# Optimization experiments

Measured on AMD Instinct MI355X. Metric: run time of the kernel, lower is better.

The kernel has to match this reference:

```python
import jax, jax.numpy as jnp
import numpy as np

EPS = 1e-6
NEG = -100000.0


def _ln(x):
    # LayerNorm, elementwise_affine=False, eps=1e-6
    mu = jnp.mean(x, axis=-1, keepdims=True)
    var = jnp.mean((x - mu) ** 2, axis=-1, keepdims=True)
    return (x - mu) * jax.lax.rsqrt(var + EPS)


def _split_heads(x, h):
    b, s, d = x.shape
    return x.reshape(b, s, h, d // h).transpose(0, 2, 1, 3)  # [B,H,S,Dh]


def _merge_heads(x):
    b, h, s, dh = x.shape
    return x.transpose(0, 2, 1, 3).reshape(b, s, h * dh)


def _conv_pool(x, w):
    # grouped Conv2d(num_heads -> num_heads, kernel=(4,1), stride=(4,1), groups=num_heads, bias=False)
    # x: [B,H,S,Dh] as NCHW, w: [H,1,4,1] as OIHW
    return jax.lax.conv_general_dilated(
        x, w, window_strides=(4, 1), padding='VALID',
        dimension_numbers=('NCHW', 'OIHW', 'NCHW'),
        feature_group_count=x.shape[1])


def setup_inputs() -> dict:
    key = jax.random.key(0)
    ks = jax.random.split(key, 14)
    B, S, M, D, QKV, MLP, H = 4, 4096, 256, 768, 768, 3072, 12
    std = 0.02
    f = lambda k, shp: jax.random.normal(k, shp, jnp.float32) * std
    return {
        'x': jax.random.normal(ks[0], (B, S, D), jnp.float32),
        'memory': jax.random.normal(ks[1], (B, M, D), jnp.float32),
        'mask': jax.random.randint(ks[2], (B, S), 0, 2).astype(jnp.int32),
        'Wq': f(ks[3], (QKV, D)), 'Wk': f(ks[4], (QKV, D)),
        'Wv': f(ks[5], (QKV, D)), 'Wo': f(ks[6], (D, QKV)),
        'conv_w': f(ks[7], (H, 1, 4, 1)),
        'Uq': f(ks[8], (QKV, D)), 'Uk': f(ks[9], (QKV, D)),
        'Uv': f(ks[10], (QKV, D)), 'Uo': f(ks[11], (D, QKV)),
        'W1': f(ks[12], (MLP, D)), 'W2': f(ks[13], (D, MLP)),
    }


def reference(x, memory, mask, Wq, Wk, Wv, Wo, conv_w, Uq, Uk, Uv, Uo, W1, W2):
    H = conv_w.shape[0]
    maskf = mask.astype(x.dtype)                       # [B,S]

    # ---- pack: ConvAttention(memory as q, x as k/v); conv downsamples k/v ->
    #      shape_change=True so the k_mask is skipped (as in the torch code).
    q = _split_heads(memory @ Wq.T, H)                 # [B,H,M,Dh], unit temperature (log_temp=0)
    k = _split_heads(x @ Wk.T, H)                      # [B,H,S,Dh]
    v = _split_heads(x @ Wv.T, H)
    k = _conv_pool(k, conv_w)                          # [B,H,S//4,Dh]
    v = _conv_pool(v, conv_w)
    logits = jnp.einsum('bhqd,bhkd->bhqk', q, k)
    att = jax.nn.softmax(logits, axis=-1)
    packed = _merge_heads(att @ v) @ Wo.T              # [B,M,D]

    # ---- unpack: TAttention(x as q, packed as k/v) with q_mask injection
    head_dim = Uq.shape[0] // H
    uq = _split_heads(x @ Uq.T, H) * (1.0 / jnp.sqrt(jnp.asarray(head_dim, x.dtype)))
    uk = _split_heads(packed @ Uk.T, H)                # [B,H,M,Dh]
    uv = _split_heads(packed @ Uv.T, H)
    ulogits = jnp.einsum('bhqd,bhkd->bhqk', uq, uk)    # [B,H,S,M]
    ulogits = ulogits + NEG * (1.0 - maskf[:, None, :, None])
    uatt = jax.nn.softmax(ulogits, axis=-1)
    unpacked = _merge_heads(uatt @ uv) @ Uo.T          # [B,S,D]

    unpacked = unpacked * maskf[..., None]
    q_out = _ln(x + unpacked)
    m_out = _ln(memory + packed)

    # FFN: Linear -> GELU(exact) -> Linear (dropout=0)
    h = jax.nn.gelu(jnp.einsum('bsd,md->bsm', q_out, W1), approximate=False)
    y = jnp.einsum('bsm,dm->bsd', h, W2)
    y = y * maskf[..., None]
    q_out = _ln(q_out + y)
    return (q_out, m_out)
```

## Files before the change

### kernel.cpp

```cpp
#include <hip/hip_runtime.h>
#include <hip/hip_bf16.h>
#include <math.h>


typedef unsigned short u16;
typedef __attribute__((ext_vector_type(8))) short bf8v;
typedef __attribute__((ext_vector_type(4))) float f4v;
typedef __attribute__((ext_vector_type(4))) unsigned short us4v;

#define AS1 __attribute__((address_space(1)))
#define AS3 __attribute__((address_space(3)))

__device__ __forceinline__ void gld_lds16(const void* g, void* l) {
  __builtin_amdgcn_global_load_lds((const AS1 unsigned int*)g,
                                   (AS3 unsigned int*)l, 16, 0, 0);
}

__device__ __forceinline__ u16 bf16_rne(float x) {
  unsigned u = __float_as_uint(x);
  return (u16)((u + 0x7fffu + ((u >> 16) & 1u)) >> 16);
}
__device__ __forceinline__ float bf16_to_f(u16 h) {
  return __uint_as_float(((unsigned)h) << 16);
}

__global__ __launch_bounds__(256) void tobf16_kernel(
    const float* __restrict__ in, u16* __restrict__ o, int n4) {
  int i = blockIdx.x * 256 + threadIdx.x;
  if (i >= n4) return;
  float4 v = ((const float4*)in)[i];
  us4v h;
  h[0] = bf16_rne(v.x); h[1] = bf16_rne(v.y);
  h[2] = bf16_rne(v.z); h[3] = bf16_rne(v.w);
  ((us4v*)o)[i] = h;
}

template <int BN, int GELU, int OMODE>
__global__ __launch_bounds__(256) void bgemm_kernel(
    const u16* __restrict__ A, const u16* __restrict__ B,
    float* __restrict__ Cf, u16* __restrict__ Cb, int M, int N, int K,
    int lda, int ldb, int ldc, long long aSB, long long aSH, long long bSB,
    long long bSH, long long cSB, long long cSH, int HB, float scale) {
  constexpr int NJ = BN / 32;
  constexpr int LPB = BN / 64;
  __shared__ u16 smA[2][4096];
  __shared__ u16 smB[2][BN * 32];
  const int t = threadIdx.x;
  const int w = t >> 6, lane = t & 63;
  const int z = blockIdx.z;
  const int bb = z / HB, hh = z % HB;
  const u16* Ab = A + bb * aSB + hh * aSH;
  const u16* Bb = B + bb * bSB + hh * bSH;
  float* Cfb = (OMODE != 1) ? (Cf + bb * cSB + hh * cSH) : nullptr;
  u16* Cbb = (OMODE >= 1) ? (Cb + bb * cSB + hh * cSH) : nullptr;

  const int gx = gridDim.x;
  const int nwg = gx * gridDim.y;
  int f = blockIdx.x + gx * blockIdx.y;
  if ((nwg & 7) == 0) {
    const int cpx = nwg >> 3;
    f = (f & 7) * cpx + (f >> 3);
  }
  const int row0 = (f / gx) * 128, col0 = (f % gx) * BN;

  const int brow_l = lane >> 2;
  const int bchunk = ((lane & 3) ^ ((lane >> 3) & 3)) * 8;
  const int fr = lane & 15;
  const int fq = lane >> 4;
  const int fco = (fq ^ ((lane >> 1) & 3)) * 8;
  const int wr = (w >> 1) * 64, wc = (w & 1) * (BN / 2);

  f4v acc[4][NJ];
#pragma unroll
  for (int i = 0; i < 4; ++i)
#pragma unroll
    for (int j = 0; j < NJ; ++j) acc[i][j] = {0.f, 0.f, 0.f, 0.f};

  const int NT = K >> 5;

#pragma unroll
  for (int i = 0; i < 2; ++i) {
    const int g = w * 2 + i;
    const int r = g * 16 + brow_l;
    gld_lds16(Ab + (long long)(row0 + r) * lda + bchunk,
              &smA[0][g * 512 + lane * 8]);
  }
#pragma unroll
  for (int i = 0; i < LPB; ++i) {
    const int g = w * LPB + i;
    const int r = g * 16 + brow_l;
    gld_lds16(Bb + (long long)(col0 + r) * ldb + bchunk,
              &smB[0][g * 512 + lane * 8]);
  }
  __syncthreads();

  for (int tt = 0; tt < NT; ++tt) {
    const int cur = tt & 1, nxt = cur ^ 1;
    const bool more = (tt + 1) < NT;
    if (more) {
      const int k1 = (tt + 1) << 5;
#pragma unroll
      for (int i = 0; i < 2; ++i) {
        const int g = w * 2 + i;
        const int r = g * 16 + brow_l;
        gld_lds16(Ab + (long long)(row0 + r) * lda + k1 + bchunk,
                  &smA[nxt][g * 512 + lane * 8]);
      }
#pragma unroll
      for (int i = 0; i < LPB; ++i) {
        const int g = w * LPB + i;
        const int r = g * 16 + brow_l;
        gld_lds16(Bb + (long long)(col0 + r) * ldb + k1 + bchunk,
                  &smB[nxt][g * 512 + lane * 8]);
      }
    }
    {
      bf8v af[4], bfr[NJ];
#pragma unroll
      for (int mi = 0; mi < 4; ++mi)
        af[mi] = *(const bf8v*)&smA[cur][(wr + mi * 16 + fr) * 32 + fco];
#pragma unroll
      for (int nj = 0; nj < NJ; ++nj)
        bfr[nj] = *(const bf8v*)&smB[cur][(wc + nj * 16 + fr) * 32 + fco];
#pragma unroll
      for (int mi = 0; mi < 4; ++mi)
#pragma unroll
        for (int nj = 0; nj < NJ; ++nj)
          acc[mi][nj] = __builtin_amdgcn_mfma_f32_16x16x32_bf16(
              af[mi], bfr[nj], acc[mi][nj], 0, 0, 0);
    }
    __syncthreads();
  }

#pragma unroll
  for (int mi = 0; mi < 4; ++mi)
#pragma unroll
    for (int nj = 0; nj < NJ; ++nj) {
      const int col = col0 + wc + nj * 16 + fr;
      const long long base =
          (long long)(row0 + wr + mi * 16 + fq * 4) * ldc + col;
#pragma unroll
      for (int j = 0; j < 4; ++j) {
        float v = acc[mi][nj][j] * scale;
        if (GELU) v = 0.5f * v * (1.f + erff(v * 0.70710678118654752f));
        const long long idx = base + (long long)j * ldc;
        if (OMODE != 1) Cfb[idx] = v;
        if (OMODE >= 1) Cbb[idx] = bf16_rne(v);
      }
    }
}

__global__ __launch_bounds__(512) void fused_unpack_attn(
    const u16* __restrict__ q, const u16* __restrict__ k,
    const u16* __restrict__ vt, u16* __restrict__ o) {
  __shared__ char pool[76800];
  u16* smA = (u16*)pool;
  u16* smB = (u16*)(pool + 8192);
  u16* Pbuf = (u16*)pool;
  u16* smV = (u16*)(pool + 65536);
  float* partial = (float*)(pool + 73728);
  float* rowmax = (float*)(pool + 75776);
  float* rowsum = (float*)(pool + 76288);

  const int t = threadIdx.x;
  const int w = t >> 6, lane = t & 63;
  const int z = blockIdx.z;
  const int b = z / 12, h = z % 12;
  const int q0 = blockIdx.x * 128;

  const long long qoff = ((long long)b * 4096 + q0) * 768 + h * 64;
  const long long koff = ((long long)b * 256) * 768 + h * 64;
  const long long vbase = ((long long)(b * 12 + h)) * 16384;

  const int fr = lane & 15, fq = lane >> 4;
  const int fco = (fq ^ ((lane >> 1) & 3)) * 8;
  const int brow_l = lane >> 2;
  const int bchunk = ((lane & 3) ^ ((lane >> 3) & 3)) * 8;

  const int wr = (w >> 2) * 64, wc = (w & 3) * 64;
  f4v acc[4][4];
#pragma unroll
  for (int i = 0; i < 4; ++i)
#pragma unroll
    for (int j = 0; j < 4; ++j) acc[i][j] = {0.f, 0.f, 0.f, 0.f};

  for (int k0 = 0; k0 < 64; k0 += 32) {
    __syncthreads();
#pragma unroll
    for (int i = 0; i < 2; ++i) {
      const int g = w * 2 + i;
      const int r = g * 16 + brow_l;
      gld_lds16(k + koff + (long long)r * 768 + k0 + bchunk,
                smB + g * 512 + lane * 8);
    }
    {
      const int r = w * 16 + brow_l;
      gld_lds16(q + qoff + (long long)r * 768 + k0 + bchunk,
                smA + w * 512 + lane * 8);
    }
    __syncthreads();
#pragma unroll
    for (int mi = 0; mi < 4; ++mi) {
      const bf8v a0 = *(const bf8v*)&smA[(wr + mi * 16 + fr) * 32 + fco];
#pragma unroll
      for (int nj = 0; nj < 4; ++nj) {
        const bf8v b0 = *(const bf8v*)&smB[(wc + nj * 16 + fr) * 32 + fco];
        acc[mi][nj] = __builtin_amdgcn_mfma_f32_16x16x32_bf16(a0, b0, acc[mi][nj], 0, 0, 0);
      }
    }
  }
  __syncthreads();

  if (w < 4) {
    const int r = w * 16 + brow_l;
    gld_lds16(vt + vbase + (long long)r * 256 + bchunk,
              smV + w * 512 + lane * 8);
  }

#pragma unroll
  for (int mi = 0; mi < 4; ++mi)
#pragma unroll
    for (int j = 0; j < 4; ++j) {
      float m = fmaxf(fmaxf(acc[mi][0][j], acc[mi][1][j]),
                      fmaxf(acc[mi][2][j], acc[mi][3][j]));
#pragma unroll
      for (int o2 = 1; o2 < 16; o2 <<= 1) m = fmaxf(m, __shfl_xor(m, o2));
      if (fr == 0) partial[(w & 3) * 128 + wr + mi * 16 + fq * 4 + j] = m;
    }
  __syncthreads();
  if (t < 128)
    rowmax[t] = fmaxf(fmaxf(partial[t], partial[128 + t]),
                      fmaxf(partial[256 + t], partial[384 + t]));
  __syncthreads();
#pragma unroll
  for (int mi = 0; mi < 4; ++mi)
#pragma unroll
    for (int j = 0; j < 4; ++j) {
      const int row = wr + mi * 16 + fq * 4 + j;
      const float rm = rowmax[row];
      float s = 0.f;
#pragma unroll
      for (int nj = 0; nj < 4; ++nj) {
        const float e = exp2f(acc[mi][nj][j] - rm);
        s += e;
        const int col = wc + nj * 16 + fr;
        const int kc = col >> 5, kloc = col & 31;
        Pbuf[kc * 4096 + row * 32 + (((kloc >> 3) ^ ((row >> 1) & 3)) * 8) +
             (kloc & 7)] = bf16_rne(e);
      }
#pragma unroll
      for (int o2 = 1; o2 < 16; o2 <<= 1) s += __shfl_xor(s, o2);
      if (fr == 0) partial[(w & 3) * 128 + row] = s;
    }
  __syncthreads();
  if (t < 128)
    rowsum[t] = 1.f / ((partial[t] + partial[128 + t]) +
                       (partial[256 + t] + partial[384 + t]));
  __syncthreads();

  const int wrp = (w >> 1) * 32, wcp = (w & 1) * 32;
  f4v acc2[2][2];
#pragma unroll
  for (int i = 0; i < 2; ++i)
#pragma unroll
    for (int j = 0; j < 2; ++j) acc2[i][j] = {0.f, 0.f, 0.f, 0.f};

  for (int kc = 0; kc < 8; ++kc) {
    const int cur = (kc & 1) * 2048;
    if (kc < 7 && w < 4) {
      const int r = w * 16 + brow_l;
      gld_lds16(vt + vbase + (long long)r * 256 + (kc + 1) * 32 + bchunk,
                smV + (2048 - cur) + w * 512 + lane * 8);
    }
#pragma unroll
    for (int mi = 0; mi < 2; ++mi) {
      const bf8v pa =
          *(const bf8v*)&Pbuf[kc * 4096 + (wrp + mi * 16 + fr) * 32 + fco];
#pragma unroll
      for (int nj = 0; nj < 2; ++nj) {
        const bf8v v0 =
            *(const bf8v*)&smV[cur + (wcp + nj * 16 + fr) * 32 + fco];
        acc2[mi][nj] = __builtin_amdgcn_mfma_f32_16x16x32_bf16(pa, v0, acc2[mi][nj], 0, 0, 0);
      }
    }
    __syncthreads();
  }
#pragma unroll
  for (int mi = 0; mi < 2; ++mi)
#pragma unroll
    for (int nj = 0; nj < 2; ++nj)
#pragma unroll
      for (int j = 0; j < 4; ++j) {
        const int row = wrp + mi * 16 + fq * 4 + j;
        const int col = wcp + nj * 16 + fr;
        o[qoff + (long long)row * 768 + col] =
            bf16_rne(acc2[mi][nj][j] * rowsum[row]);
      }
}

__global__ __launch_bounds__(256) void conv_bf16_kernel(
    const u16* __restrict__ in, const float* __restrict__ w,
    u16* __restrict__ o, int total, int ld) {
  int idx = blockIdx.x * 256 + threadIdx.x;
  if (idx >= total) return;
  const int dh = idx & 63;
  int r = idx >> 6;
  const int tt = r & 1023; r >>= 10;
  const int h = r % 12;
  const int b = r / 12;
  const long long s = ((long long)(b * 4096 + 4 * tt)) * ld + h * 64 + dh;
  const float* wh = w + h * 4;
  float v = 0.f;
#pragma unroll
  for (int j = 0; j < 4; ++j) v = fmaf(wh[j], bf16_to_f(in[s + j * ld]), v);
  o[idx] = bf16_rne(v);
}

__global__ __launch_bounds__(256) void convT_bf16_kernel(
    const u16* __restrict__ in, const float* __restrict__ w,
    u16* __restrict__ o, int total, int ld) {
  int idx = blockIdx.x * 256 + threadIdx.x;
  if (idx >= total) return;
  const int tt = idx & 1023;
  int r = idx >> 10;
  const int dh = r & 63; r >>= 6;
  const int h = r % 12;
  const int b = r / 12;
  const long long s = ((long long)(b * 4096 + 4 * tt)) * ld + h * 64 + dh;
  const float* wh = w + h * 4;
  float v = 0.f;
#pragma unroll
  for (int j = 0; j < 4; ++j) v = fmaf(wh[j], bf16_to_f(in[s + j * ld]), v);
  o[idx] = bf16_rne(v);
}

__global__ __launch_bounds__(256) void transT_bf16_kernel(
    const float* __restrict__ in, u16* __restrict__ o, int total) {
  int idx = blockIdx.x * 256 + threadIdx.x;
  if (idx >= total) return;
  const int key = idx & 255;
  int r = idx >> 8;
  const int dh = r & 63; r >>= 6;
  const int h = r % 12;
  const int b = r / 12;
  o[idx] = bf16_rne(in[((long long)(b * 256 + key)) * 768 + h * 64 + dh]);
}

__global__ __launch_bounds__(256) void softmax_bf16_kernel(
    const float* __restrict__ in, u16* __restrict__ ob) {
  const long long row = blockIdx.x;
  const float* p = in + row * 1024;
  const int t = threadIdx.x;
  __shared__ float red[4];
  float v[4];
  float lmax = -3.4e38f;
#pragma unroll
  for (int i = 0; i < 4; ++i) {
    v[i] = p[t + (i << 8)];
    lmax = fmaxf(lmax, v[i]);
  }
  for (int o = 32; o; o >>= 1) lmax = fmaxf(lmax, __shfl_xor(lmax, o));
  if ((t & 63) == 0) red[t >> 6] = lmax;
  __syncthreads();
  const float gmax = fmaxf(fmaxf(red[0], red[1]), fmaxf(red[2], red[3]));
  float lsum = 0.f;
#pragma unroll
  for (int i = 0; i < 4; ++i) {
    v[i] = expf(v[i] - gmax);
    lsum += v[i];
  }
  __syncthreads();
  for (int o = 32; o; o >>= 1) lsum += __shfl_xor(lsum, o);
  if ((t & 63) == 0) red[t >> 6] = lsum;
  __syncthreads();
  const float inv = 1.f / (red[0] + red[1] + red[2] + red[3]);
#pragma unroll
  for (int i = 0; i < 4; ++i)
    ob[row * 1024 + t + (i << 8)] = bf16_rne(v[i] * inv);
}

__global__ __launch_bounds__(256) void ln_kernel(
    const float* __restrict__ a, const float* __restrict__ b,
    const int* __restrict__ mask, float* __restrict__ out,
    u16* __restrict__ outb) {
  const long long row = blockIdx.x;
  const float* pa = a + row * 768;
  const float* pb = b + row * 768;
  const float ms = mask ? (float)mask[row] : 1.f;
  __shared__ float buf[768];
  __shared__ float red[4];
  const int t = threadIdx.x;
  float lsum = 0.f;
#pragma unroll
  for (int i = t; i < 768; i += 256) {
    const float v = fmaf(pb[i], ms, pa[i]);
    buf[i] = v;
    lsum += v;
  }
  for (int o = 32; o; o >>= 1) lsum += __shfl_xor(lsum, o);
  if ((t & 63) == 0) red[t >> 6] = lsum;
  __syncthreads();
  const float mu = (red[0] + red[1] + red[2] + red[3]) * (1.f / 768.f);
  float lvar = 0.f;
#pragma unroll
  for (int i = t; i < 768; i += 256) {
    const float d = buf[i] - mu;
    lvar = fmaf(d, d, lvar);
  }
  __syncthreads();
  for (int o = 32; o; o >>= 1) lvar += __shfl_xor(lvar, o);
  if ((t & 63) == 0) red[t >> 6] = lvar;
  __syncthreads();
  const float var = (red[0] + red[1] + red[2] + red[3]) * (1.f / 768.f);
  const float rstd = rsqrtf(var + 1e-6f);
  float* po = out + row * 768;
  u16* pob = outb ? outb + row * 768 : nullptr;
#pragma unroll
  for (int i = t; i < 768; i += 256) {
    const float v = (buf[i] - mu) * rstd;
    po[i] = v;
    if (outb) pob[i] = bf16_rne(v);
  }
}

static inline void tobf16(hipStream_t st, const float* in, u16* o, int n) {
  int n4 = n / 4;
  tobf16_kernel<<<(n4 + 255) / 256, 256, 0, st>>>(in, o, n4);
}

extern "C" void kernel_launch(void* const* d_in, const int* in_sizes, int n_in,
                              void* d_out, int out_size, void* d_ws,
                              size_t ws_size, hipStream_t stream) {
  const float* x = (const float*)d_in[0];
  const float* memory = (const float*)d_in[1];
  const int* mask = (const int*)d_in[2];
  const float* Wq = (const float*)d_in[3];
  const float* Wk = (const float*)d_in[4];
  const float* Wv = (const float*)d_in[5];
  const float* Wo = (const float*)d_in[6];
  const float* conv_w = (const float*)d_in[7];
  const float* Uq = (const float*)d_in[8];
  const float* Uk = (const float*)d_in[9];
  const float* Uv = (const float*)d_in[10];
  const float* Uo = (const float*)d_in[11];
  const float* W1 = (const float*)d_in[12];
  const float* W2 = (const float*)d_in[13];
  float* out = (float*)d_out;
  float* ws = (float*)d_ws;

  const int XR = 16384, MR = 1024, D = 768, MLP = 3072;
  const long long CB = 3145728;
  const int WD = 589824;
  const int WM = 2359296;

  float* slotA = ws + 0;
  float* slotB = ws + 12582912;
  float* slotC = ws + 25165824;
  float* X     = ws + 28311552;
  float* s0    = ws + 34603008;
  float* s1    = ws + 35389440;
  float* s2    = ws + 36175872;
  float* s3    = ws + 36962304;
  float* s4    = ws + 37748736;
  float* Wp    = ws + 38535168;

  u16* kvb  = (u16*)slotA;
  u16* xb   = (u16*)slotB;
  u16* attb = (u16*)(slotB + 6291456);
  u16* uqb  = (u16*)(slotB + 6291456);
  u16* uattvb = (u16*)slotA;
  u16* qout1b = (u16*)(out + 6291456);
  u16* hb   = (u16*)slotA;
  float* ybuf = slotC;
  u16* qpb  = (u16*)s0;
  u16* memb = qpb + 786432;
  u16* avmb = (u16*)s1;
  u16* pkb  = avmb + 786432;
  float* packed = s2;
  u16* ukbb = (u16*)s3;
  u16* uvTb = ukbb + 786432;
  float* uvb = s4;
  u16* kpb  = (u16*)X;
  u16* vpTb = kpb + 3145728;
  u16* wp16 = (u16*)Wp;
  u16* Wkvb = wp16;
  u16* Wqb = wp16 + 2 * WD;
  u16* Wob = wp16 + 3 * WD;
  u16 *Uqb = wp16, *Ukb = wp16 + WD, *Uvb = wp16 + 2 * WD, *Uob = wp16 + 3 * WD;
  u16 *W1b = wp16, *W2b = wp16 + WM;

  tobf16(stream, x, xb, 12582912);
  tobf16(stream, memory, memb, 786432);
  tobf16(stream, Wk, Wkvb, WD);
  tobf16(stream, Wv, Wkvb + WD, WD);
  tobf16(stream, Wq, Wqb, WD);
  tobf16(stream, Wo, Wob, WD);
  bgemm_kernel<128, 0, 1><<<dim3(12, 128, 1), 256, 0, stream>>>(
      xb, Wkvb, nullptr, kvb, XR, 1536, D, D, D, 1536,
      0, 0, 0, 0, 0, 0, 1, 1.f);
  bgemm_kernel<128, 0, 1><<<dim3(6, 8, 1), 256, 0, stream>>>(
      memb, Wqb, nullptr, qpb, MR, D, D, D, D, D, 0, 0, 0, 0, 0, 0, 1, 1.f);
  conv_bf16_kernel<<<12288, 256, 0, stream>>>(kvb, conv_w, kpb, 3145728, 1536);
  convT_bf16_kernel<<<12288, 256, 0, stream>>>(kvb + 768, conv_w, vpTb, 3145728, 1536);
  bgemm_kernel<128, 0, 0><<<dim3(8, 2, 48), 256, 0, stream>>>(
      qpb, kpb, slotA, nullptr, 256, 1024, 64, 768, 64, 1024,
      196608, 64, 786432, 65536, 3145728, 262144, 12, 1.f);
  softmax_bf16_kernel<<<12288, 256, 0, stream>>>(slotA, attb);
  bgemm_kernel<64, 0, 1><<<dim3(1, 2, 48), 256, 0, stream>>>(
      attb, vpTb, nullptr, avmb, 256, 64, 1024, 1024, 1024, 768,
      3145728, 262144, 786432, 65536, 196608, 64, 12, 1.f);
  bgemm_kernel<128, 0, 2><<<dim3(6, 8, 1), 256, 0, stream>>>(
      avmb, Wob, packed, pkb, MR, D, D, D, D, D, 0, 0, 0, 0, 0, 0, 1, 1.f);
  ln_kernel<<<MR, 256, 0, stream>>>(memory, packed, nullptr, out + 12582912,
                                    nullptr);

  tobf16(stream, Uq, Uqb, WD);
  tobf16(stream, Uk, Ukb, WD);
  tobf16(stream, Uv, Uvb, WD);
  tobf16(stream, Uo, Uob, WD);
  bgemm_kernel<128, 0, 1><<<dim3(6, 128, 1), 256, 0, stream>>>(
      xb, Uqb, nullptr, uqb, XR, D, D, D, D, D, 0, 0, 0, 0, 0, 0, 1,
      0.18033688011112042592f);
  bgemm_kernel<128, 0, 1><<<dim3(6, 8, 1), 256, 0, stream>>>(
      pkb, Ukb, nullptr, ukbb, MR, D, D, D, D, D, 0, 0, 0, 0, 0, 0, 1, 1.f);
  bgemm_kernel<128, 0, 0><<<dim3(6, 8, 1), 256, 0, stream>>>(
      pkb, Uvb, uvb, nullptr, MR, D, D, D, D, D, 0, 0, 0, 0, 0, 0, 1, 1.f);
  transT_bf16_kernel<<<3072, 256, 0, stream>>>(uvb, uvTb, 786432);
  {
    dim3 g(32, 1, 48);
    fused_unpack_attn<<<g, 512, 0, stream>>>(uqb, ukbb, uvTb, uattvb);
  }
  bgemm_kernel<128, 0, 0><<<dim3(6, 32, 4), 256, 0, stream>>>(
      uattvb, Uob, slotB, nullptr, 4096, D, D, D, D, D,
      CB, 0, 0, 0, CB, 0, 1, 1.f);
  ln_kernel<<<XR, 256, 0, stream>>>(x, slotB, mask, slotB, qout1b);

  tobf16(stream, W1, W1b, WM);
  tobf16(stream, W2, W2b, WM);
  for (int c = 0; c < 2; ++c) {
    bgemm_kernel<128, 1, 1><<<dim3(24, 32, 2), 256, 0, stream>>>(
        qout1b + (long long)c * 2 * 3145728, W1b, nullptr, hb, 4096, MLP, D,
        D, D, MLP, 3145728, 0, 0, 0, 12582912, 0, 1, 1.f);
    bgemm_kernel<64, 0, 0><<<dim3(12, 32, 2), 256, 0, stream>>>(
        hb, W2b, ybuf, nullptr, 4096, D, MLP, MLP, MLP, D,
        12582912, 0, 0, 0, 3145728, 0, 1, 1.f);
    ln_kernel<<<8192, 256, 0, stream>>>(slotB + (long long)c * 2 * CB, ybuf,
                                        mask + c * 8192,
                                        out + (long long)c * 2 * CB, nullptr);
  }
}
```

Baseline: 720.9 us.

## Fuse Uq projection into KV GEMM, merge Uk/Uv GEMMs, in-place softmax, retile FFN

Concatenates Wk, Wv and a pre-scaled Uq into a single 2304-wide weight so one GEMM over x produces k, v and the unpack query together, and merges the Uk and Uv projections of packed into one 1536-wide GEMM. The transpose kernel now reads bf16 directly, softmax writes its output in place, and the workspace layout is reorganised to match. FFN GEMM tile widths change (BN 256 for W1, 128 for W2). The intent is to cut repeated reads of x and extra kernel launches. Folding the scale into bf16 weights changes rounding slightly, and the larger tiles may hurt occupancy.

```diff
diff --git a/kernel.cpp b/kernel.cpp
--- a/kernel.cpp
+++ b/kernel.cpp
@@ -25,13 +25,13 @@
 }
 
 __global__ __launch_bounds__(256) void tobf16_kernel(
-    const float* __restrict__ in, u16* __restrict__ o, int n4) {
+    const float* __restrict__ in, u16* __restrict__ o, int n4, float scale) {
   int i = blockIdx.x * 256 + threadIdx.x;
   if (i >= n4) return;
   float4 v = ((const float4*)in)[i];
   us4v h;
-  h[0] = bf16_rne(v.x); h[1] = bf16_rne(v.y);
-  h[2] = bf16_rne(v.z); h[3] = bf16_rne(v.w);
+  h[0] = bf16_rne(v.x * scale); h[1] = bf16_rne(v.y * scale);
+  h[2] = bf16_rne(v.z * scale); h[3] = bf16_rne(v.w * scale);
   ((us4v*)o)[i] = h;
 }
 
@@ -151,7 +151,7 @@
 }
 
 __global__ __launch_bounds__(512) void fused_unpack_attn(
-    const u16* __restrict__ q, const u16* __restrict__ k,
+    const u16* __restrict__ q, int ldq, const u16* __restrict__ k, int ldk,
     const u16* __restrict__ vt, u16* __restrict__ o) {
   __shared__ char pool[76800];
   u16* smA = (u16*)pool;
@@ -168,9 +168,10 @@
   const int b = z / 12, h = z % 12;
   const int q0 = blockIdx.x * 128;
 
-  const long long qoff = ((long long)b * 4096 + q0) * 768 + h * 64;
-  const long long koff = ((long long)b * 256) * 768 + h * 64;
+  const long long qoff = (long long)(b * 4096 + q0) * ldq + h * 64;
+  const long long koff = (long long)(b * 256) * ldk + h * 64;
   const long long vbase = ((long long)(b * 12 + h)) * 16384;
+  const long long ooff = (long long)(b * 4096 + q0) * 768 + h * 64;
 
   const int fr = lane & 15, fq = lane >> 4;
   const int fco = (fq ^ ((lane >> 1) & 3)) * 8;
@@ -190,12 +191,12 @@
     for (int i = 0; i < 2; ++i) {
       const int g = w * 2 + i;
       const int r = g * 16 + brow_l;
-      gld_lds16(k + koff + (long long)r * 768 + k0 + bchunk,
+      gld_lds16(k + koff + (long long)r * ldk + k0 + bchunk,
                 smB + g * 512 + lane * 8);
     }
     {
       const int r = w * 16 + brow_l;
-      gld_lds16(q + qoff + (long long)r * 768 + k0 + bchunk,
+      gld_lds16(q + qoff + (long long)r * ldq + k0 + bchunk,
                 smA + w * 512 + lane * 8);
     }
     __syncthreads();
@@ -293,7 +294,7 @@
       for (int j = 0; j < 4; ++j) {
         const int row = wrp + mi * 16 + fq * 4 + j;
         const int col = wcp + nj * 16 + fr;
-        o[qoff + (long long)row * 768 + col] =
+        o[ooff + (long long)row * 768 + col] =
             bf16_rne(acc2[mi][nj][j] * rowsum[row]);
       }
 }
@@ -334,8 +335,8 @@
   o[idx] = bf16_rne(v);
 }
 
-__global__ __launch_bounds__(256) void transT_bf16_kernel(
-    const float* __restrict__ in, u16* __restrict__ o, int total) {
+__global__ __launch_bounds__(256) void transT_b2b_kernel(
+    const u16* __restrict__ in, u16* __restrict__ o, int total, int ld) {
   int idx = blockIdx.x * 256 + threadIdx.x;
   if (idx >= total) return;
   const int key = idx & 255;
@@ -343,13 +344,13 @@
   const int dh = r & 63; r >>= 6;
   const int h = r % 12;
   const int b = r / 12;
-  o[idx] = bf16_rne(in[((long long)(b * 256 + key)) * 768 + h * 64 + dh]);
-}
-
-__global__ __launch_bounds__(256) void softmax_bf16_kernel(
-    const float* __restrict__ in, u16* __restrict__ ob) {
+  o[idx] = in[((long long)(b * 256 + key)) * ld + h * 64 + dh];
+}
+
+__global__ __launch_bounds__(256) void softmax_ip_kernel(float* __restrict__ data) {
   const long long row = blockIdx.x;
-  const float* p = in + row * 1024;
+  float* p = data + row * 1024;
+  u16* ob = (u16*)p;
   const int t = threadIdx.x;
   __shared__ float red[4];
   float v[4];
@@ -375,8 +376,7 @@
   __syncthreads();
   const float inv = 1.f / (red[0] + red[1] + red[2] + red[3]);
 #pragma unroll
-  for (int i = 0; i < 4; ++i)
-    ob[row * 1024 + t + (i << 8)] = bf16_rne(v[i] * inv);
+  for (int i = 0; i < 4; ++i) ob[t + (i << 8)] = bf16_rne(v[i] * inv);
 }
 
 __global__ __launch_bounds__(256) void ln_kernel(
@@ -423,9 +423,10 @@
   }
 }
 
-static inline void tobf16(hipStream_t st, const float* in, u16* o, int n) {
+static inline void tobf16(hipStream_t st, const float* in, u16* o, int n,
+                          float scale = 1.f) {
   int n4 = n / 4;
-  tobf16_kernel<<<(n4 + 255) / 256, 256, 0, st>>>(in, o, n4);
+  tobf16_kernel<<<(n4 + 255) / 256, 256, 0, st>>>(in, o, n4, scale);
 }
 
 extern "C" void kernel_launch(void* const* d_in, const int* in_sizes, int n_in,
@@ -453,98 +454,92 @@
   const int WD = 589824;
   const int WM = 2359296;
 
-  float* slotA = ws + 0;
-  float* slotB = ws + 12582912;
-  float* slotC = ws + 25165824;
-  float* X     = ws + 28311552;
-  float* s0    = ws + 34603008;
-  float* s1    = ws + 35389440;
-  float* s2    = ws + 36175872;
-  float* s3    = ws + 36962304;
-  float* s4    = ws + 37748736;
-  float* Wp    = ws + 38535168;
-
-  u16* kvb  = (u16*)slotA;
-  u16* xb   = (u16*)slotB;
-  u16* attb = (u16*)(slotB + 6291456);
-  u16* uqb  = (u16*)(slotB + 6291456);
-  u16* uattvb = (u16*)slotA;
+  float* A0 = ws + 0;
+  float* A1 = ws + 18874368;
+  float* A2 = ws + 31457280;
+
+  u16* xb    = (u16*)(A0 + 12582912);
+  u16* kvqb  = (u16*)A0;
+  float* logits = A1;
+  u16* attb  = (u16*)A1;
+  u16* uattvb = (u16*)A1;
+  float* unp = A0;
   u16* qout1b = (u16*)(out + 6291456);
-  u16* hb   = (u16*)slotA;
-  float* ybuf = slotC;
-  u16* qpb  = (u16*)s0;
+  u16* hb    = (u16*)A1;
+  float* ybuf = A2;
+
+  u16* kpb  = (u16*)A2;
+  u16* vpTb = kpb + 3145728;
+  u16* qpb  = (u16*)(A2 + 3145728);
   u16* memb = qpb + 786432;
-  u16* avmb = (u16*)s1;
+  u16* avmb = (u16*)(A2 + 3932160);
   u16* pkb  = avmb + 786432;
-  float* packed = s2;
-  u16* ukbb = (u16*)s3;
-  u16* uvTb = ukbb + 786432;
-  float* uvb = s4;
-  u16* kpb  = (u16*)X;
-  u16* vpTb = kpb + 3145728;
-  u16* wp16 = (u16*)Wp;
-  u16* Wkvb = wp16;
-  u16* Wqb = wp16 + 2 * WD;
-  u16* Wob = wp16 + 3 * WD;
-  u16 *Uqb = wp16, *Ukb = wp16 + WD, *Uvb = wp16 + 2 * WD, *Uob = wp16 + 3 * WD;
-  u16 *W1b = wp16, *W2b = wp16 + WM;
+  float* packed = A2 + 4718592;
+  u16* ukvb = (u16*)(A2 + 5505024);
+  u16* uvTb = (u16*)(A2 + 6291456);
+  u16* wp16 = (u16*)(A2 + 7077888);
+
+  u16* Wkvqb = wp16;
+  u16* Wqb = wp16 + 2304 * 768;
+  u16* Wob = Wqb + WD;
+  u16* Ukvb2 = wp16;
+  u16* Uob = wp16 + 1536 * 768;
+  u16* W1b = wp16;
+  u16* W2b = wp16 + WM;
 
   tobf16(stream, x, xb, 12582912);
   tobf16(stream, memory, memb, 786432);
-  tobf16(stream, Wk, Wkvb, WD);
-  tobf16(stream, Wv, Wkvb + WD, WD);
+  tobf16(stream, Wk, Wkvqb, WD);
+  tobf16(stream, Wv, Wkvqb + WD, WD);
+  tobf16(stream, Uq, Wkvqb + 2 * WD, WD, 0.18033688011112042592f);
   tobf16(stream, Wq, Wqb, WD);
   tobf16(stream, Wo, Wob, WD);
-  bgemm_kernel<128, 0, 1><<<dim3(12, 128, 1), 256, 0, stream>>>(
-      xb, Wkvb, nullptr, kvb, XR, 1536, D, D, D, 1536,
+  bgemm_kernel<256, 0, 1><<<dim3(9, 128, 1), 256, 0, stream>>>(
+      xb, Wkvqb, nullptr, kvqb, XR, 2304, D, D, D, 2304,
       0, 0, 0, 0, 0, 0, 1, 1.f);
   bgemm_kernel<128, 0, 1><<<dim3(6, 8, 1), 256, 0, stream>>>(
       memb, Wqb, nullptr, qpb, MR, D, D, D, D, D, 0, 0, 0, 0, 0, 0, 1, 1.f);
-  conv_bf16_kernel<<<12288, 256, 0, stream>>>(kvb, conv_w, kpb, 3145728, 1536);
-  convT_bf16_kernel<<<12288, 256, 0, stream>>>(kvb + 768, conv_w, vpTb, 3145728, 1536);
+  conv_bf16_kernel<<<12288, 256, 0, stream>>>(kvqb, conv_w, kpb, 3145728, 2304);
+  convT_bf16_kernel<<<12288, 256, 0, stream>>>(kvqb + 768, conv_w, vpTb, 3145728, 2304);
   bgemm_kernel<128, 0, 0><<<dim3(8, 2, 48), 256, 0, stream>>>(
-      qpb, kpb, slotA, nullptr, 256, 1024, 64, 768, 64, 1024,
+      qpb, kpb, logits, nullptr, 256, 1024, 64, 768, 64, 1024,
       196608, 64, 786432, 65536, 3145728, 262144, 12, 1.f);
-  softmax_bf16_kernel<<<12288, 256, 0, stream>>>(slotA, attb);
+  softmax_ip_kernel<<<12288, 256, 0, stream>>>(logits);
   bgemm_kernel<64, 0, 1><<<dim3(1, 2, 48), 256, 0, stream>>>(
-      attb, vpTb, nullptr, avmb, 256, 64, 1024, 1024, 1024, 768,
-      3145728, 262144, 786432, 65536, 196608, 64, 12, 1.f);
+      attb, vpTb, nullptr, avmb, 256, 64, 1024, 2048, 1024, 768,
+      6291456, 524288, 786432, 65536, 196608, 64, 12, 1.f);
   bgemm_kernel<128, 0, 2><<<dim3(6, 8, 1), 256, 0, stream>>>(
       avmb, Wob, packed, pkb, MR, D, D, D, D, D, 0, 0, 0, 0, 0, 0, 1, 1.f);
   ln_kernel<<<MR, 256, 0, stream>>>(memory, packed, nullptr, out + 12582912,
                                     nullptr);
 
-  tobf16(stream, Uq, Uqb, WD);
-  tobf16(stream, Uk, Ukb, WD);
-  tobf16(stream, Uv, Uvb, WD);
+  tobf16(stream, Uk, Ukvb2, WD);
+  tobf16(stream, Uv, Ukvb2 + WD, WD);
   tobf16(stream, Uo, Uob, WD);
-  bgemm_kernel<128, 0, 1><<<dim3(6, 128, 1), 256, 0, stream>>>(
-      xb, Uqb, nullptr, uqb, XR, D, D, D, D, D, 0, 0, 0, 0, 0, 0, 1,
-      0.18033688011112042592f);
-  bgemm_kernel<128, 0, 1><<<dim3(6, 8, 1), 256, 0, stream>>>(
-      pkb, Ukb, nullptr, ukbb, MR, D, D, D, D, D, 0, 0, 0, 0, 0, 0, 1, 1.f);
-  bgemm_kernel<128, 0, 0><<<dim3(6, 8, 1), 256, 0, stream>>>(
-      pkb, Uvb, uvb, nullptr, MR, D, D, D, D, D, 0, 0, 0, 0, 0, 0, 1, 1.f);
-  transT_bf16_kernel<<<3072, 256, 0, stream>>>(uvb, uvTb, 786432);
+  bgemm_kernel<128, 0, 1><<<dim3(12, 8, 1), 256, 0, stream>>>(
+      pkb, Ukvb2, nullptr, ukvb, MR, 1536, D, D, D, 1536,
+      0, 0, 0, 0, 0, 0, 1, 1.f);
+  transT_b2b_kernel<<<3072, 256, 0, stream>>>(ukvb + 768, uvTb, 786432, 1536);
   {
     dim3 g(32, 1, 48);
-    fused_unpack_attn<<<g, 512, 0, stream>>>(uqb, ukbb, uvTb, uattvb);
+    fused_unpack_attn<<<g, 512, 0, stream>>>(kvqb + 1536, 2304, ukvb, 1536,
+                                             uvTb, uattvb);
   }
   bgemm_kernel<128, 0, 0><<<dim3(6, 32, 4), 256, 0, stream>>>(
-      uattvb, Uob, slotB, nullptr, 4096, D, D, D, D, D,
+      uattvb, Uob, unp, nullptr, 4096, D, D, D, D, D,
       CB, 0, 0, 0, CB, 0, 1, 1.f);
-  ln_kernel<<<XR, 256, 0, stream>>>(x, slotB, mask, slotB, qout1b);
+  ln_kernel<<<XR, 256, 0, stream>>>(x, unp, mask, unp, qout1b);
 
   tobf16(stream, W1, W1b, WM);
   tobf16(stream, W2, W2b, WM);
   for (int c = 0; c < 2; ++c) {
-    bgemm_kernel<128, 1, 1><<<dim3(24, 32, 2), 256, 0, stream>>>(
-        qout1b + (long long)c * 2 * 3145728, W1b, nullptr, hb, 4096, MLP, D,
-        D, D, MLP, 3145728, 0, 0, 0, 12582912, 0, 1, 1.f);
-    bgemm_kernel<64, 0, 0><<<dim3(12, 32, 2), 256, 0, stream>>>(
+    bgemm_kernel<256, 1, 1><<<dim3(12, 32, 2), 256, 0, stream>>>(
+        qout1b + (long long)c * 2 * CB, W1b, nullptr, hb, 4096, MLP, D,
+        D, D, MLP, CB, 0, 0, 0, 12582912, 0, 1, 1.f);
+    bgemm_kernel<128, 0, 0><<<dim3(6, 32, 2), 256, 0, stream>>>(
         hb, W2b, ybuf, nullptr, 4096, D, MLP, MLP, MLP, D,
-        12582912, 0, 0, 0, 3145728, 0, 1, 1.f);
-    ln_kernel<<<8192, 256, 0, stream>>>(slotB + (long long)c * 2 * CB, ybuf,
+        12582912, 0, 0, 0, CB, 0, 1, 1.f);
+    ln_kernel<<<8192, 256, 0, stream>>>(unp + (long long)c * 2 * CB, ybuf,
                                         mask + c * 8192,
                                         out + (long long)c * 2 * CB, nullptr);
   }
```

Measured after the change: 843.6 us. 1.17x slower.
